# Kernel optimization log

Measured on AMD Instinct MI355X. Metric: run time of the kernel, lower is better.

Reference implementation:

```python
import jax, jax.numpy as jnp
import numpy as np

NORM_EPS = 1e-6   # config.norm_eps
MAG_EPS = 1e-6    # config.magnitude_eps


def setup_inputs() -> dict:
    key = jax.random.key(0)
    k0, k1, k2, k3, k4, k5 = jax.random.split(key, 6)
    B, S, IN, OUT, R, L = 4, 2048, 2048, 2048, 4, 16
    x = jax.random.normal(k0, (B, S, IN), dtype=jnp.float32)
    # frozen quantization indices (buffer _indices), values in [0, lut_size)
    indices = jax.random.randint(k1, (OUT, IN), 0, L, dtype=jnp.int32)
    # monotonic LUT in [-1, 1] (make_lut with include_zero=False)
    lut = jnp.linspace(-1.0, 1.0, L, dtype=jnp.float32)
    scale_A = jax.random.normal(k2, (OUT, R), dtype=jnp.float32)
    scale_B = jax.random.normal(k3, (R, IN), dtype=jnp.float32)
    rank_magnitude = jax.random.uniform(k4, (R,), dtype=jnp.float32)
    bias = jax.random.normal(k5, (OUT,), dtype=jnp.float32) * 0.01
    return {"x": x, "indices": indices, "lut": lut, "scale_A": scale_A,
            "scale_B": scale_B, "rank_magnitude": rank_magnitude, "bias": bias}


def reference(x, indices, lut, scale_A, scale_B, rank_magnitude, bias):
    # _get_normalized_scales: force_positive_scales='abs', magnitude_activation='softplus'
    A = jnp.abs(scale_A)                                            # [out, r]
    A_dir = A / jnp.maximum(jnp.linalg.norm(A, axis=0, keepdims=True), NORM_EPS)
    Bm = jnp.abs(scale_B)                                           # [r, in]
    B_dir = Bm / jnp.maximum(jnp.linalg.norm(Bm, axis=1, keepdims=True), NORM_EPS)
    g = jax.nn.softplus(rank_magnitude) + MAG_EPS                   # [r]
    # LUT dequant: Q = lut[_indices], [out, in]
    Q = lut[indices]
    # rank-by-rank forward: y = sum_k g_k * (a_k \odot (Q (b_k \odot x))) + bias
    # t[b,s,r,o] = sum_i x[b,s,i] * B_dir[r,i] * Q[o,i]
    t = jnp.einsum('bsi,ri,oi->bsro', x, B_dir, Q)
    y = jnp.einsum('bsro,or,r->bso', t, A_dir, g) + bias
    return y
```

## Files before the change

kernel.cpp:

```cpp
#include <hip/hip_runtime.h>

#define IN_DIM  2048
#define OUT_DIM 2048
#define MROWS   8192
#define RANK    4

typedef unsigned short ushort_t;
typedef __attribute__((ext_vector_type(8))) short  short8;
typedef __attribute__((ext_vector_type(4))) float  floatx4;

__device__ __forceinline__ unsigned short f2bf(float f) {
  union { float f; unsigned int u; } v; v.f = f;
  unsigned int r = v.u + 0x7fffu + ((v.u >> 16) & 1u);
  return (unsigned short)(r >> 16);
}

__device__ __forceinline__ void gload16(const ushort_t* g, short* l) {
  __builtin_amdgcn_global_load_lds(
      (const __attribute__((address_space(1))) void*)g,
      (__attribute__((address_space(3))) void*)l, 16, 0, 0);
}

__global__ void coef_kernel(const float* __restrict__ sA, const float* __restrict__ sB,
                            const float* __restrict__ mag, float* __restrict__ cOut) {
  __shared__ float part[8][256];
  __shared__ float tot[8];
  int t = threadIdx.x;
  float sa[4] = {0.f, 0.f, 0.f, 0.f};
  for (int o = t; o < OUT_DIM; o += 256) {
    float4 v = *(const float4*)(sA + o * 4);
    sa[0] += v.x * v.x; sa[1] += v.y * v.y; sa[2] += v.z * v.z; sa[3] += v.w * v.w;
  }
  float sb[4] = {0.f, 0.f, 0.f, 0.f};
  for (int r = 0; r < 4; ++r)
    for (int i = t; i < IN_DIM; i += 256) { float v = sB[r * IN_DIM + i]; sb[r] += v * v; }
  for (int q = 0; q < 4; ++q) { part[q][t] = sa[q]; part[4 + q][t] = sb[q]; }
  __syncthreads();
  if (t < 8) { float s = 0.f; for (int j = 0; j < 256; ++j) s += part[t][j]; tot[t] = s; }
  __syncthreads();
  if (t < 4) {
    float g  = log1pf(expf(mag[t])) + 1e-6f;
    float na = fmaxf(sqrtf(tot[t]),     1e-6f);
    float nb = fmaxf(sqrtf(tot[4 + t]), 1e-6f);
    cOut[t] = g / (na * nb);
  }
}

__global__ void build_w_kernel(const int* __restrict__ idx, const float* __restrict__ lut,
                               const float* __restrict__ sA, const float* __restrict__ sB,
                               const float* __restrict__ c, ushort_t* __restrict__ W) {
  __shared__ float aA[4];
  __shared__ float lutS[16];
  int o = blockIdx.x;
  int t = threadIdx.x;
  if (t < 4)  aA[t]   = fabsf(sA[o * 4 + t]) * c[t];
  if (t < 16) lutS[t] = lut[t];
  __syncthreads();
  int i = t * 8;
  const int* ip = idx + (size_t)o * IN_DIM + i;
  unsigned short u[8];
  #pragma unroll
  for (int j = 0; j < 8; ++j) {
    float s = aA[0] * fabsf(sB[0 * IN_DIM + i + j])
            + aA[1] * fabsf(sB[1 * IN_DIM + i + j])
            + aA[2] * fabsf(sB[2 * IN_DIM + i + j])
            + aA[3] * fabsf(sB[3 * IN_DIM + i + j]);
    u[j] = f2bf(lutS[ip[j]] * s);
  }
  uint4 o4;
  o4.x = (unsigned)u[0] | ((unsigned)u[1] << 16);
  o4.y = (unsigned)u[2] | ((unsigned)u[3] << 16);
  o4.z = (unsigned)u[4] | ((unsigned)u[5] << 16);
  o4.w = (unsigned)u[6] | ((unsigned)u[7] << 16);
  *(uint4*)(W + (size_t)o * IN_DIM + i) = o4;
}

__global__ void cast_kernel(const float* __restrict__ x, ushort_t* __restrict__ xb) {
  size_t i = ((size_t)blockIdx.x * 256 + threadIdx.x) * 8;
  float4 a = *(const float4*)(x + i);
  float4 b = *(const float4*)(x + i + 4);
  uint4 o4;
  o4.x = (unsigned)f2bf(a.x) | ((unsigned)f2bf(a.y) << 16);
  o4.y = (unsigned)f2bf(a.z) | ((unsigned)f2bf(a.w) << 16);
  o4.z = (unsigned)f2bf(b.x) | ((unsigned)f2bf(b.y) << 16);
  o4.w = (unsigned)f2bf(b.z) | ((unsigned)f2bf(b.w) << 16);
  *(uint4*)(xb + i) = o4;
}

__global__ __launch_bounds__(256) void gemm_kernel(const ushort_t* __restrict__ A,
                                                   const ushort_t* __restrict__ W,
                                                   const float* __restrict__ bias,
                                                   float* __restrict__ C) {
  __shared__ short As[128 * 32];
  __shared__ short Bs[128 * 32];
  const int t    = threadIdx.x;
  const int lane = t & 63;
  const int wid  = t >> 6;
  const int wr   = wid >> 1;
  const int wc   = wid & 1;
  const int rowBase = blockIdx.y * 128;
  const int colBase = blockIdx.x * 128;

  floatx4 acc[4][4];
  #pragma unroll
  for (int i = 0; i < 4; ++i)
    #pragma unroll
    for (int j = 0; j < 4; ++j) acc[i][j] = (floatx4){0.f, 0.f, 0.f, 0.f};

  const int j0 = t, j1 = t + 256;
  const ushort_t* a0 = A + (size_t)(rowBase + (j0 >> 2)) * IN_DIM + (j0 & 3) * 8;
  const ushort_t* a1 = A + (size_t)(rowBase + (j1 >> 2)) * IN_DIM + (j1 & 3) * 8;
  const ushort_t* b0 = W + (size_t)(colBase + (j0 >> 2)) * IN_DIM + (j0 & 3) * 8;
  const ushort_t* b1 = W + (size_t)(colBase + (j1 >> 2)) * IN_DIM + (j1 & 3) * 8;
  short* lA0 = As + (wid * 64) * 8;
  short* lA1 = As + (256 + wid * 64) * 8;
  short* lB0 = Bs + (wid * 64) * 8;
  short* lB1 = Bs + (256 + wid * 64) * 8;

  const int rA   = lane & 15;
  const int kOff = (lane >> 4) * 8;

  for (int k0 = 0; k0 < IN_DIM; k0 += 32) {
    gload16(a0 + k0, lA0);
    gload16(a1 + k0, lA1);
    gload16(b0 + k0, lB0);
    gload16(b1 + k0, lB1);
    __syncthreads();

    short8 af[4], bf[4];
    #pragma unroll
    for (int mi = 0; mi < 4; ++mi)
      af[mi] = *(const short8*)(As + (wr * 64 + mi * 16 + rA) * 32 + kOff);
    #pragma unroll
    for (int ni = 0; ni < 4; ++ni)
      bf[ni] = *(const short8*)(Bs + (wc * 64 + ni * 16 + rA) * 32 + kOff);
    #pragma unroll
    for (int mi = 0; mi < 4; ++mi)
      #pragma unroll
      for (int ni = 0; ni < 4; ++ni)
        acc[mi][ni] = __builtin_amdgcn_mfma_f32_16x16x32_bf16(af[mi], bf[ni], acc[mi][ni], 0, 0, 0);
    __syncthreads();
  }

  const int mB = rowBase + wr * 64 + (lane >> 4) * 4;
  const int nB = colBase + wc * 64 + (lane & 15);
  #pragma unroll
  for (int ni = 0; ni < 4; ++ni) {
    float bv = bias[nB + ni * 16];
    #pragma unroll
    for (int mi = 0; mi < 4; ++mi)
      #pragma unroll
      for (int r = 0; r < 4; ++r)
        C[(size_t)(mB + mi * 16 + r) * OUT_DIM + (nB + ni * 16)] = acc[mi][ni][r] + bv;
  }
}

extern "C" void kernel_launch(void* const* d_in, const int* in_sizes, int n_in,
                              void* d_out, int out_size, void* d_ws, size_t ws_size,
                              hipStream_t stream) {
  const float* x    = (const float*)d_in[0];
  const int*   idx  = (const int*)d_in[1];
  const float* lut  = (const float*)d_in[2];
  const float* sA   = (const float*)d_in[3];
  const float* sB   = (const float*)d_in[4];
  const float* mag  = (const float*)d_in[5];
  const float* bias = (const float*)d_in[6];
  float* y = (float*)d_out;

  char* ws = (char*)d_ws;
  float*    c  = (float*)ws;
  ushort_t* W  = (ushort_t*)(ws + 256);
  ushort_t* xb = (ushort_t*)(ws + 256 + (size_t)OUT_DIM * IN_DIM * 2);

  coef_kernel<<<1, 256, 0, stream>>>(sA, sB, mag, c);
  build_w_kernel<<<OUT_DIM, 256, 0, stream>>>(idx, lut, sA, sB, c, W);
  cast_kernel<<<(MROWS * IN_DIM) / (256 * 8), 256, 0, stream>>>(x, xb);
  dim3 g(OUT_DIM / 128, MROWS / 128);
  gemm_kernel<<<g, 256, 0, stream>>>(xb, W, bias, y);
}
```

Measured before the change: 248.6 us.

## Swizzle GEMM LDS tiles and merge cast and weight-build kernels

Result: faster. 243.1 us (-2.2%).

```diff
diff --git a/kernel.cpp b/kernel.cpp
--- a/kernel.cpp
+++ b/kernel.cpp
@@ -46,45 +46,48 @@
   }
 }
 
-__global__ void build_w_kernel(const int* __restrict__ idx, const float* __restrict__ lut,
-                               const float* __restrict__ sA, const float* __restrict__ sB,
-                               const float* __restrict__ c, ushort_t* __restrict__ W) {
-  __shared__ float aA[4];
-  __shared__ float lutS[16];
-  int o = blockIdx.x;
+__global__ void prep_kernel(const float* __restrict__ x, ushort_t* __restrict__ xb,
+                            const int* __restrict__ idx, const float* __restrict__ lut,
+                            const float* __restrict__ sA, const float* __restrict__ sB,
+                            const float* __restrict__ c, ushort_t* __restrict__ W) {
   int t = threadIdx.x;
-  if (t < 4)  aA[t]   = fabsf(sA[o * 4 + t]) * c[t];
-  if (t < 16) lutS[t] = lut[t];
-  __syncthreads();
-  int i = t * 8;
-  const int* ip = idx + (size_t)o * IN_DIM + i;
-  unsigned short u[8];
-  #pragma unroll
-  for (int j = 0; j < 8; ++j) {
-    float s = aA[0] * fabsf(sB[0 * IN_DIM + i + j])
-            + aA[1] * fabsf(sB[1 * IN_DIM + i + j])
-            + aA[2] * fabsf(sB[2 * IN_DIM + i + j])
-            + aA[3] * fabsf(sB[3 * IN_DIM + i + j]);
-    u[j] = f2bf(lutS[ip[j]] * s);
+  if (blockIdx.x < 8192) {
+    size_t i = ((size_t)blockIdx.x * 256 + t) * 8;
+    float4 a = *(const float4*)(x + i);
+    float4 b = *(const float4*)(x + i + 4);
+    uint4 o4;
+    o4.x = (unsigned)f2bf(a.x) | ((unsigned)f2bf(a.y) << 16);
+    o4.y = (unsigned)f2bf(a.z) | ((unsigned)f2bf(a.w) << 16);
+    o4.z = (unsigned)f2bf(b.x) | ((unsigned)f2bf(b.y) << 16);
+    o4.w = (unsigned)f2bf(b.z) | ((unsigned)f2bf(b.w) << 16);
+    *(uint4*)(xb + i) = o4;
+  } else {
+    __shared__ float aA[4];
+    __shared__ float lutS[16];
+    int o = blockIdx.x - 8192;
+    if (t < 4)  aA[t]   = fabsf(sA[o * 4 + t]) * c[t];
+    if (t < 16) lutS[t] = lut[t];
+    __syncthreads();
+    int i = t * 8;
+    const int4* ip4 = (const int4*)(idx + (size_t)o * IN_DIM + i);
+    int4 i0 = ip4[0], i1 = ip4[1];
+    int ii[8] = {i0.x, i0.y, i0.z, i0.w, i1.x, i1.y, i1.z, i1.w};
+    unsigned short u[8];
+    #pragma unroll
+    for (int j = 0; j < 8; ++j) {
+      float s = aA[0] * fabsf(sB[0 * IN_DIM + i + j])
+              + aA[1] * fabsf(sB[1 * IN_DIM + i + j])
+              + aA[2] * fabsf(sB[2 * IN_DIM + i + j])
+              + aA[3] * fabsf(sB[3 * IN_DIM + i + j]);
+      u[j] = f2bf(lutS[ii[j]] * s);
+    }
+    uint4 o4;
+    o4.x = (unsigned)u[0] | ((unsigned)u[1] << 16);
+    o4.y = (unsigned)u[2] | ((unsigned)u[3] << 16);
+    o4.z = (unsigned)u[4] | ((unsigned)u[5] << 16);
+    o4.w = (unsigned)u[6] | ((unsigned)u[7] << 16);
+    *(uint4*)(W + (size_t)o * IN_DIM + i) = o4;
   }
-  uint4 o4;
-  o4.x = (unsigned)u[0] | ((unsigned)u[1] << 16);
-  o4.y = (unsigned)u[2] | ((unsigned)u[3] << 16);
-  o4.z = (unsigned)u[4] | ((unsigned)u[5] << 16);
-  o4.w = (unsigned)u[6] | ((unsigned)u[7] << 16);
-  *(uint4*)(W + (size_t)o * IN_DIM + i) = o4;
-}
-
-__global__ void cast_kernel(const float* __restrict__ x, ushort_t* __restrict__ xb) {
-  size_t i = ((size_t)blockIdx.x * 256 + threadIdx.x) * 8;
-  float4 a = *(const float4*)(x + i);
-  float4 b = *(const float4*)(x + i + 4);
-  uint4 o4;
-  o4.x = (unsigned)f2bf(a.x) | ((unsigned)f2bf(a.y) << 16);
-  o4.y = (unsigned)f2bf(a.z) | ((unsigned)f2bf(a.w) << 16);
-  o4.z = (unsigned)f2bf(b.x) | ((unsigned)f2bf(b.y) << 16);
-  o4.w = (unsigned)f2bf(b.z) | ((unsigned)f2bf(b.w) << 16);
-  *(uint4*)(xb + i) = o4;
 }
 
 __global__ __launch_bounds__(256) void gemm_kernel(const ushort_t* __restrict__ A,
@@ -107,18 +110,21 @@
     #pragma unroll
     for (int j = 0; j < 4; ++j) acc[i][j] = (floatx4){0.f, 0.f, 0.f, 0.f};
 
-  const int j0 = t, j1 = t + 256;
-  const ushort_t* a0 = A + (size_t)(rowBase + (j0 >> 2)) * IN_DIM + (j0 & 3) * 8;
-  const ushort_t* a1 = A + (size_t)(rowBase + (j1 >> 2)) * IN_DIM + (j1 & 3) * 8;
-  const ushort_t* b0 = W + (size_t)(colBase + (j0 >> 2)) * IN_DIM + (j0 & 3) * 8;
-  const ushort_t* b1 = W + (size_t)(colBase + (j1 >> 2)) * IN_DIM + (j1 & 3) * 8;
+  const int row0 = t >> 2;
+  const int c0   = t & 3;
+  const int kc0  = c0 ^ ((row0 >> 1) & 3);
+  const ushort_t* a0 = A + (size_t)(rowBase + row0) * IN_DIM + kc0 * 8;
+  const ushort_t* a1 = A + (size_t)(rowBase + row0 + 64) * IN_DIM + kc0 * 8;
+  const ushort_t* b0 = W + (size_t)(colBase + row0) * IN_DIM + kc0 * 8;
+  const ushort_t* b1 = W + (size_t)(colBase + row0 + 64) * IN_DIM + kc0 * 8;
   short* lA0 = As + (wid * 64) * 8;
   short* lA1 = As + (256 + wid * 64) * 8;
   short* lB0 = Bs + (wid * 64) * 8;
   short* lB1 = Bs + (256 + wid * 64) * 8;
 
   const int rA   = lane & 15;
-  const int kOff = (lane >> 4) * 8;
+  const int slot = ((rA >> 1) & 3) ^ (lane >> 4);
+  const int kOff = slot * 8;
 
   for (int k0 = 0; k0 < IN_DIM; k0 += 32) {
     gload16(a0 + k0, lA0);
@@ -173,8 +179,7 @@
   ushort_t* xb = (ushort_t*)(ws + 256 + (size_t)OUT_DIM * IN_DIM * 2);
 
   coef_kernel<<<1, 256, 0, stream>>>(sA, sB, mag, c);
-  build_w_kernel<<<OUT_DIM, 256, 0, stream>>>(idx, lut, sA, sB, c, W);
-  cast_kernel<<<(MROWS * IN_DIM) / (256 * 8), 256, 0, stream>>>(x, xb);
+  prep_kernel<<<8192 + OUT_DIM, 256, 0, stream>>>(x, xb, idx, lut, sA, sB, c, W);
   dim3 g(OUT_DIM / 128, MROWS / 128);
   gemm_kernel<<<g, 256, 0, stream>>>(xb, W, bias, y);
 }
```
